# Performance work log

Measured on AMD Instinct MI355X. Metric: run time of the kernel, lower is better.

## Reference

```python
import jax, jax.numpy as jnp
import numpy as np

N, D, E = 100000, 128, 1600000
C = 1.0
MIN_NORM = 1e-15   # hgcn min_norm clamp
BALL_EPS = 4e-3    # float32 eps for proj onto Poincare ball


def artanh(x):
    # hgcn Artanh clamps input away from +-1 (use 1e-7, the fp32-representable analog of 1e-15)
    return jnp.arctanh(jnp.clip(x, -1.0 + 1e-7, 1.0 - 1e-7))


def _norm(x):
    return jnp.maximum(jnp.linalg.norm(x, axis=-1, keepdims=True), MIN_NORM)


def proj(x, c):
    norm = _norm(x)
    maxnorm = (1.0 - BALL_EPS) / jnp.sqrt(c)
    return jnp.where(norm > maxnorm, x / norm * maxnorm, x)


def expmap0(u, c):
    sc = jnp.sqrt(c)
    n = _norm(u)
    return jnp.tanh(sc * n) * u / (sc * n)


def logmap0(p, c):
    sc = jnp.sqrt(c)
    n = _norm(p)
    return artanh(sc * n) * p / (sc * n)


def mobius_add(x, y, c):
    x2 = jnp.sum(x * x, -1, keepdims=True)
    y2 = jnp.sum(y * y, -1, keepdims=True)
    xy = jnp.sum(x * y, -1, keepdims=True)
    num = (1.0 + 2.0 * c * xy + c * y2) * x + (1.0 - c * x2) * y
    den = 1.0 + 2.0 * c * xy + c * c * x2 * y2
    return num / jnp.maximum(den, MIN_NORM)


def mobius_matvec(m, x, c):
    sc = jnp.sqrt(c)
    xn = _norm(x)
    mx = x @ m.T
    mxn = _norm(mx)
    res = jnp.tanh(mxn / xn * artanh(sc * xn)) * mx / (mxn * sc)
    zero = jnp.all(mx == 0, axis=-1, keepdims=True)
    return jnp.where(zero, jnp.zeros_like(res), res)


def hgc_layer(x, edge_index, edge_weight, w, b, c_in, c_out, n):
    # HypLinear: mobius matvec + hyperbolic bias
    h = proj(mobius_matvec(w, x, c_in), c_in)
    hyp_b = proj(expmap0(b[None, :], c_in), c_in)
    h = proj(mobius_add(h, hyp_b, c_in), c_in)
    # HypAgg: aggregate in tangent space via sparse adjacency (spmm)
    xt = logmap0(h, c_in)                                   # [N, D]
    msg = xt[edge_index[1]] * edge_weight[:, None]          # [E, D]
    agg = jax.ops.segment_sum(msg, edge_index[0], num_segments=n)
    h = proj(expmap0(agg, c_in), c_in)
    # HypAct: relu in tangent space, re-map to ball at c_out
    xt = jax.nn.relu(logmap0(h, c_in))
    return proj(expmap0(xt, c_out), c_out)


def setup_inputs() -> dict:
    key = jax.random.key(0)
    ks = jax.random.split(key, 8)
    x = jax.random.normal(ks[0], (N, D), dtype=jnp.float32)
    edge_index = jax.random.randint(ks[1], (2, E), 0, N, dtype=jnp.int64 if jax.config.jax_enable_x64 else jnp.int32)
    edge_weight = jax.random.uniform(ks[2], (E,), dtype=jnp.float32)
    s = 1.0 / np.sqrt(D)
    w1 = jax.random.normal(ks[3], (D, D), dtype=jnp.float32) * s
    b1 = jax.random.normal(ks[4], (D,), dtype=jnp.float32) * s
    w2 = jax.random.normal(ks[5], (D, D), dtype=jnp.float32) * s
    b2 = jax.random.normal(ks[6], (D,), dtype=jnp.float32) * s
    return {"x": x, "edge_index": edge_index, "edge_weight": edge_weight,
            "w1": w1, "b1": b1, "w2": w2, "b2": b2}


def reference(x, edge_index, edge_weight, w1, b1, w2, b2):
    c = jnp.float32(C)
    n = x.shape[0]
    # encode(): proj_tan0 is identity on the Poincare ball
    xh = proj(expmap0(x, c), c)
    h = hgc_layer(xh, edge_index, edge_weight, w1, b1, c, c, n)
    h = hgc_layer(h, edge_index, edge_weight, w2, b2, c, c, n)
    return h
```

## Files before the change

kernel.cpp:

```cpp
#include <hip/hip_runtime.h>
#include <math.h>
#include <stdint.h>

#define D 128
#define MAXNORM (1.0f - 4e-3f)
#define ART_CLAMP 0.9999999f
#define BKT_BITS 7
#define BKT_NODES 128
#define BKT_CAP 4096
#define NB_ROWN 1024

typedef __attribute__((ext_vector_type(8))) short short8;
typedef __attribute__((ext_vector_type(4))) float float4v;
typedef __attribute__((ext_vector_type(4))) int intv4;

__device__ __forceinline__ float waveAllReduce(float v) {
#pragma unroll
    for (int off = 32; off; off >>= 1) v += __shfl_xor(v, off, 64);
    return v;
}

__device__ __forceinline__ float reduce16(float v) {
    v += __shfl_xor(v, 8, 64);
    v += __shfl_xor(v, 4, 64);
    v += __shfl_xor(v, 2, 64);
    v += __shfl_xor(v, 1, 64);
    return v;
}

__device__ __forceinline__ uint16_t f2bf(float f) {
    uint32_t u = __float_as_uint(f);
    uint32_t r = u + 0x7FFFu + ((u >> 16) & 1u);
    return (uint16_t)(r >> 16);
}
__device__ __forceinline__ float bf2f(uint16_t b) {
    return __uint_as_float((uint32_t)b << 16);
}

__device__ __forceinline__ float rcpf(float x) { return __builtin_amdgcn_rcpf(x); }
__device__ __forceinline__ float fsqrtf(float x) { return __builtin_amdgcn_sqrtf(x); }
__device__ __forceinline__ float fast_tanh(float x) {
    float e = __expf(2.0f * x);
    float t = 1.0f - 2.0f * rcpf(e + 1.0f);
    return (x < 1e-4f) ? x : t;
}
__device__ __forceinline__ float fast_atanh(float x) {
    float t = 0.5f * __logf((1.0f + x) * rcpf(1.0f - x));
    return (x < 1e-4f) ? x : t;
}


#define CS_STRIDE 136

struct GemmLds {
    short8 Ah[2][16][16];
    short8 Al[2][16][16];
    float Cs[16 * CS_STRIDE];
};
struct BinLds { int cnt[1024]; int base[1024]; };
struct SortLds { int cnt[BKT_NODES]; int cur[BKT_NODES]; int2 buf[BKT_CAP]; };
union LdsBG { GemmLds g; BinLds b; };
union LdsSG { GemmLds g; SortLds s; };


__device__ __forceinline__ void rowNorms_body(int bid, int tid,
                                              const float* __restrict__ X,
                                              float* __restrict__ XN, int n) {
    int lane = tid & 63;
    int wv = (bid * 256 + tid) >> 6;
    const int nw = (NB_ROWN * 256) >> 6;
    for (int r = wv; r < n; r += nw) {
        float2 v = *(const float2*)(X + (size_t)r * D + lane * 2);
        float nn = sqrtf(waveAllReduce(v.x * v.x + v.y * v.y));
        if (lane == 0) XN[r] = nn;
    }
}

__device__ __forceinline__ void histo_body(int bid, int tid,
                                           const int* __restrict__ DST,
                                           int* __restrict__ bcnt, int E, int B,
                                           int* cnt) {
    for (int i = tid; i < B; i += 256) cnt[i] = 0;
    __syncthreads();
    int start = bid * 8192;
    int endE = min(start + 8192, E);
    for (int e = start + tid; e < endE; e += 256)
        atomicAdd(&cnt[DST[e] >> BKT_BITS], 1);
    __syncthreads();
    for (int i = tid; i < B; i += 256)
        if (cnt[i]) atomicAdd(&bcnt[i], cnt[i]);
}

__device__ __forceinline__ void prepW_body(int bid, int tid,
                                           const float* __restrict__ W1,
                                           const float* __restrict__ W2,
                                           uint16_t* __restrict__ Whi1,
                                           uint16_t* __restrict__ Wlo1,
                                           uint16_t* __restrict__ Whi2,
                                           uint16_t* __restrict__ Wlo2) {
    int i = bid * 256 + tid;
    float a1 = W1[i];
    uint16_t h1 = f2bf(a1);
    Whi1[i] = h1;
    Wlo1[i] = f2bf(a1 - bf2f(h1));
    float a2 = W2[i];
    uint16_t h2 = f2bf(a2);
    Whi2[i] = h2;
    Wlo2[i] = f2bf(a2 - bf2f(h2));
}

__device__ __forceinline__ void bias_body(int bid, int tid,
                                          const float* __restrict__ B1,
                                          const float* __restrict__ B2,
                                          float* __restrict__ HBOUT) {
    if (tid >= 64) return;
    int lane = tid;
    const float* Bp = bid ? B2 : B1;
    float v0 = Bp[lane], v1 = Bp[lane + 64];
    float nn = fmaxf(sqrtf(waveAllReduce(v0 * v0 + v1 * v1)), 1e-15f);
    float t = tanhf(nn);
    float sc = t / nn;
    float pn = fmaxf(t, 1e-15f);
    if (pn > MAXNORM) sc *= MAXNORM / pn;
    HBOUT[bid * D + lane] = v0 * sc;
    HBOUT[bid * D + lane + 64] = v1 * sc;
}

__device__ __forceinline__ void binEdges_body(int bid, int tid,
                                              const int* __restrict__ DST,
                                              const int* __restrict__ SRC,
                                              const float* __restrict__ EW,
                                              int* __restrict__ gcur,
                                              int2* __restrict__ binned, int E, int B,
                                              int* cnt, int* base) {
    int start = bid * 8192;
    int endE = min(start + 8192, E);
    for (int i = tid; i < B; i += 256) cnt[i] = 0;
    __syncthreads();
    for (int e = start + tid; e < endE; e += 256)
        atomicAdd(&cnt[DST[e] >> BKT_BITS], 1);
    __syncthreads();
    for (int i = tid; i < B; i += 256) {
        int c = cnt[i];
        base[i] = (c > 0) ? atomicAdd(&gcur[i], c) : 0;
        cnt[i] = 0;
    }
    __syncthreads();
    for (int e = start + tid; e < endE; e += 256) {
        int d = DST[e];
        int bk = d >> BKT_BITS;
        int r = atomicAdd(&cnt[bk], 1);
        binned[base[bk] + r] =
            make_int2(SRC[e] | ((d & (BKT_NODES - 1)) << 24), __float_as_int(EW[e]));
    }
}

__device__ __forceinline__ void sort_body(int b, int tid,
                                          int2* __restrict__ binned,
                                          const int* __restrict__ boff,
                                          int* __restrict__ rp, int n,
                                          int* cnt, int* cur, int2* buf) {
    int beg = boff[b], end = boff[b + 1];
    if (tid < BKT_NODES) cnt[tid] = 0;
    __syncthreads();
    for (int e = beg + tid; e < end; e += 256)
        atomicAdd(&cnt[((uint32_t)binned[e].x) >> 24], 1);
    __syncthreads();
    int v = (tid < BKT_NODES) ? cnt[tid] : 0;
    if (tid < BKT_NODES) cur[tid] = v;
    __syncthreads();
    for (int off = 1; off < BKT_NODES; off <<= 1) {
        int t = (tid < BKT_NODES && tid >= off) ? cur[tid - off] : 0;
        __syncthreads();
        if (tid < BKT_NODES) cur[tid] += t;
        __syncthreads();
    }
    if (tid < BKT_NODES) {
        int ex = cur[tid] - v;
        int g = b * BKT_NODES + tid;
        if (g < n) rp[g] = beg + ex;
        cur[tid] = ex;
    }
    __syncthreads();
    for (int e = beg + tid; e < end; e += 256) {
        int2 pr = binned[e];
        int dl = ((uint32_t)pr.x) >> 24;
        int pos = atomicAdd(&cur[dl], 1);
        if (pos < BKT_CAP) buf[pos] = make_int2(pr.x & 0x00FFFFFF, pr.y);
    }
    __syncthreads();
    int cnt_tot = end - beg;
    for (int i = tid; i < cnt_tot && i < BKT_CAP; i += 256)
        binned[beg + i] = buf[i];
}


__device__ __forceinline__ void split8(const float* v, short8* hi, short8* lo) {
    union { uint32_t u[4]; short8 s; } H, L;
#pragma unroll
    for (int i = 0; i < 4; i++) {
        uint16_t h0 = f2bf(v[2 * i]), h1 = f2bf(v[2 * i + 1]);
        uint16_t l0 = f2bf(v[2 * i] - bf2f(h0));
        uint16_t l1 = f2bf(v[2 * i + 1] - bf2f(h1));
        H.u[i] = (uint32_t)h0 | ((uint32_t)h1 << 16);
        L.u[i] = (uint32_t)l0 | ((uint32_t)l1 << 16);
    }
    *hi = H.s;
    *lo = L.s;
}

template <bool ENCODE>
__device__ __forceinline__ void gemm_body(int gbid, int rowOff, int tid,
                                          const float* __restrict__ A,
                                          const uint16_t* __restrict__ Whi,
                                          const uint16_t* __restrict__ Wlo,
                                          const float* __restrict__ XN,
                                          const float* __restrict__ HB,
                                          uint16_t* __restrict__ XT, int n,
                                          GemmLds* L) {
    int lane = tid & 63;
    int wv = tid >> 6;
    int tx = lane & 15;
    int q = lane >> 4;
    int sw = tx & 7;
    int row0 = rowOff + gbid * 64;

    short8 wh[2][4], wl[2][4];
#pragma unroll
    for (int c = 0; c < 2; c++) {
        int wrow = 16 * (2 * wv + c) + tx;
        const uint16_t* ph = Whi + (size_t)wrow * D + q * 8;
        const uint16_t* pl = Wlo + (size_t)wrow * D + q * 8;
#pragma unroll
        for (int t = 0; t < 4; t++) {
            wh[c][t] = *(const short8*)(ph + t * 32);
            wl[c][t] = *(const short8*)(pl + t * 32);
        }
    }

    float hbf[8];
#pragma unroll
    for (int c = 0; c < 8; c++) hbf[c] = HB[16 * c + tx];
    float hbsq = 0.f;
#pragma unroll
    for (int c = 0; c < 8; c++) hbsq += hbf[c] * hbf[c];
    float hb2 = reduce16(hbsq);

    auto loadA = [&](int tau, float4& v0, float4& v1) {
        int gr = row0 + tau * 16 + tx;
        if (gr >= n) gr = n - 1;
        const float4* ap = (const float4*)(A + (size_t)gr * D + wv * 32 + q * 8);
        v0 = ap[0];
        v1 = ap[1];
    };
    auto splitStore = [&](int b, float4 v0, float4 v1) {
        float v[8] = {v0.x, v0.y, v0.z, v0.w, v1.x, v1.y, v1.z, v1.w};
        short8 hi, lo;
        split8(v, &hi, &lo);
        int pch = (4 * wv + q) ^ sw;
        L->Ah[b][tx][pch] = hi;
        L->Al[b][tx][pch] = lo;
    };

    float4 pa0, pa1;
    loadA(0, pa0, pa1);
    splitStore(0, pa0, pa1);
    loadA(1, pa0, pa1);
    __syncthreads();

#pragma unroll
    for (int tau = 0; tau < 4; tau++) {
        int b = tau & 1;
        float4v acc[2];
        acc[0] = (float4v){0.f, 0.f, 0.f, 0.f};
        acc[1] = (float4v){0.f, 0.f, 0.f, 0.f};
#pragma unroll
        for (int t = 0; t < 4; t++) {
            int pch = (4 * t + q) ^ sw;
            short8 ahi = L->Ah[b][tx][pch];
            short8 alo = L->Al[b][tx][pch];
#pragma unroll
            for (int c = 0; c < 2; c++) {
                acc[c] = __builtin_amdgcn_mfma_f32_16x16x32_bf16(ahi, wh[c][t], acc[c], 0, 0, 0);
                acc[c] = __builtin_amdgcn_mfma_f32_16x16x32_bf16(ahi, wl[c][t], acc[c], 0, 0, 0);
                acc[c] = __builtin_amdgcn_mfma_f32_16x16x32_bf16(alo, wh[c][t], acc[c], 0, 0, 0);
            }
        }

#pragma unroll
        for (int c = 0; c < 2; c++) {
            int col = 16 * (2 * wv + c) + tx;
#pragma unroll
            for (int p = 0; p < 4; p++) {
                int lr = 4 * q + p;
                L->Cs[lr * CS_STRIDE + ((col + 4 * lr) & 127)] = acc[c][p];
            }
        }

        if (tau < 3) {
            splitStore(b ^ 1, pa0, pa1);
            if (tau < 2) loadA(tau + 2, pa0, pa1);
        }
        __syncthreads();

        int lr = 4 * wv + q;
        int row = row0 + tau * 16 + lr;
        if (row < n) {
            float y[8];
#pragma unroll
            for (int c = 0; c < 8; c++)
                y[c] = L->Cs[lr * CS_STRIDE + ((16 * c + tx + 4 * lr) & 127)];

            float s = 0.f;
#pragma unroll
            for (int c = 0; c < 8; c++) s += y[c] * y[c];
            float yn2 = reduce16(s);
            float sc, xns;
            if (ENCODE) {
                float nn = fmaxf(XN[row], 1e-15f);
                float t = fast_tanh(nn);
                sc = t * rcpf(nn);
                float pn = fmaxf(t, 1e-15f);
                if (pn > MAXNORM) { sc *= MAXNORM * rcpf(pn); pn = MAXNORM; }
                xns = pn;
            } else {
                sc = 1.0f;
                xns = fmaxf(XN[row], 1e-15f);
            }
            float mxn2 = sc * sc * yn2;
            float mxn = fmaxf(fsqrtf(mxn2), 1e-15f);
            float arg = (mxn * rcpf(xns)) * fast_atanh(fminf(xns, ART_CLAMP));
            float t = fast_tanh(arg);
            float s2 = (mxn2 == 0.0f) ? 0.0f : (sc * t * rcpf(mxn));
            float h[8];
#pragma unroll
            for (int c = 0; c < 8; c++) h[c] = y[c] * s2;
            float rn = fmaxf(t, 1e-15f);
            float hn = rn;
            if (rn > MAXNORM) {
                float f = MAXNORM * rcpf(rn);
#pragma unroll
                for (int c = 0; c < 8; c++) h[c] *= f;
                hn = MAXNORM;
            }
            float x2 = hn * hn;
            float d0 = 0.f;
#pragma unroll
            for (int c = 0; c < 8; c++) d0 += h[c] * hbf[c];
            float xy = reduce16(d0);
            float k1 = 1.0f + 2.0f * xy + hb2;
            float k2 = 1.0f - x2;
            float den = fmaxf(1.0f + 2.0f * xy + x2 * hb2, 1e-15f);
            float rden = rcpf(den);
            float av[8];
            float s3 = 0.f;
#pragma unroll
            for (int c = 0; c < 8; c++) {
                av[c] = (k1 * h[c] + k2 * hbf[c]) * rden;
                s3 += av[c] * av[c];
            }
            float an = fmaxf(fsqrtf(reduce16(s3)), 1e-15f);
            float fproj = 1.0f;
            if (an > MAXNORM) { fproj = MAXNORM * rcpf(an); an = MAXNORM; }
            float lm = fproj * fast_atanh(fminf(an, ART_CLAMP)) * rcpf(an);
            uint16_t* o = XT + (size_t)row * D + tx;
#pragma unroll
            for (int c = 0; c < 8; c++) o[16 * c] = f2bf(av[c] * lm);
        }
        __syncthreads();
    }
}


__global__ __launch_bounds__(256) void fusedPre(
    const float* __restrict__ X, float* __restrict__ XN, int n,
    const int* __restrict__ DST, int* __restrict__ bcnt, int E, int B, int gH,
    const float* __restrict__ W1, const float* __restrict__ W2,
    uint16_t* __restrict__ Whi1, uint16_t* __restrict__ Wlo1,
    uint16_t* __restrict__ Whi2, uint16_t* __restrict__ Wlo2,
    const float* __restrict__ B1, const float* __restrict__ B2,
    float* __restrict__ HBOUT) {
    __shared__ int cnt[1024];
    int bid = blockIdx.x, tid = threadIdx.x;
    if (bid < NB_ROWN) {
        rowNorms_body(bid, tid, X, XN, n);
    } else if (bid < NB_ROWN + gH) {
        histo_body(bid - NB_ROWN, tid, DST, bcnt, E, B, cnt);
    } else if (bid < NB_ROWN + gH + 64) {
        prepW_body(bid - NB_ROWN - gH, tid, W1, W2, Whi1, Wlo1, Whi2, Wlo2);
    } else {
        bias_body(bid - NB_ROWN - gH - 64, tid, B1, B2, HBOUT);
    }
}

__global__ __launch_bounds__(1024) void bucketScan(const int* __restrict__ bcnt,
                                                   int* __restrict__ boff,
                                                   int* __restrict__ gcur,
                                                   int* __restrict__ rp_last,
                                                   int B, int E) {
    __shared__ int sd[1024];
    int tid = threadIdx.x;
    int v = (tid < B) ? bcnt[tid] : 0;
    sd[tid] = v;
    __syncthreads();
    for (int off = 1; off < 1024; off <<= 1) {
        int t = (tid >= off) ? sd[tid - off] : 0;
        __syncthreads();
        sd[tid] += t;
        __syncthreads();
    }
    int ex = sd[tid] - v;
    if (tid < B) { boff[tid] = ex; gcur[tid] = ex; }
    if (tid == 0) { boff[B] = E; *rp_last = E; }
}

__global__ __launch_bounds__(256, 3) void fusedBinGemm(
    const int* __restrict__ DST, const int* __restrict__ SRC,
    const float* __restrict__ EW, int* __restrict__ gcur,
    int2* __restrict__ binned, int E, int B, int gBin,
    const float* __restrict__ A, const uint16_t* __restrict__ Whi,
    const uint16_t* __restrict__ Wlo, const float* __restrict__ XN,
    const float* __restrict__ HB, uint16_t* __restrict__ XT, int n) {
    __shared__ LdsBG u;
    int bid = blockIdx.x, tid = threadIdx.x;
    if (bid < gBin)
        binEdges_body(bid, tid, DST, SRC, EW, gcur, binned, E, B, u.b.cnt, u.b.base);
    else
        gemm_body<true>(bid - gBin, 0, tid, A, Whi, Wlo, XN, HB, XT, n, &u.g);
}

__global__ __launch_bounds__(256, 3) void fusedSortGemm(
    int2* __restrict__ binned, const int* __restrict__ boff,
    int* __restrict__ rp, int n, int gSort,
    const float* __restrict__ A, const uint16_t* __restrict__ Whi,
    const uint16_t* __restrict__ Wlo, const float* __restrict__ XN,
    const float* __restrict__ HB, uint16_t* __restrict__ XT, int rowOff) {
    __shared__ LdsSG u;
    int bid = blockIdx.x, tid = threadIdx.x;
    if (bid < gSort)
        sort_body(bid, tid, binned, boff, rp, n, u.s.cnt, u.s.cur, u.s.buf);
    else
        gemm_body<true>(bid - gSort, rowOff, tid, A, Whi, Wlo, XN, HB, XT, n, &u.g);
}

template <bool ENCODE>
__global__ __launch_bounds__(256, 3) void gemmM(const float* __restrict__ A,
                                                const uint16_t* __restrict__ Whi,
                                                const uint16_t* __restrict__ Wlo,
                                                const float* __restrict__ XN,
                                                const float* __restrict__ HB,
                                                uint16_t* __restrict__ XT, int n) {
    __shared__ GemmLds L;
    gemm_body<ENCODE>(blockIdx.x, 0, threadIdx.x, A, Whi, Wlo, XN, HB, XT, n, &L);
}


template <bool STORE_HN>
__global__ __launch_bounds__(256) void aggC(const uint16_t* __restrict__ XT,
                                            const int* __restrict__ rp,
                                            const int2* __restrict__ sorted,
                                            float* __restrict__ OUT,
                                            float* __restrict__ HN, int n) {
    int tid = threadIdx.x;
    int lane = tid & 63;
    int q = lane >> 4;
    int tx = lane & 15;
    int wv = (blockIdx.x * 256 + tid) >> 6;
    int g = wv * 4 + q;
    bool valid = (g < n);
    int gc = valid ? g : (n - 1);
    uint32_t beg = (uint32_t)rp[gc];
    uint32_t end = valid ? (uint32_t)rp[gc + 1] : beg;
    uint32_t deg = end - beg;

    int m = (int)deg;
    m = max(m, __shfl_xor(m, 16, 64));
    m = max(m, __shfl_xor(m, 32, 64));
    int ms = __builtin_amdgcn_readfirstlane(m);

    const char* sbase = (const char*)sorted;
    const char* xbase = (const char*)XT;
    uint32_t txoff = (uint32_t)tx * 16u;
    uint32_t jb = beg * 8u;
    uint32_t jendb = end * 8u;
    uint32_t jlastb = (jendb > 0u) ? (jendb - 8u) : 0u;

    float a[8];
#pragma unroll
    for (int c = 0; c < 8; c++) a[c] = 0.f;

    int2 e0 = *(const int2*)(sbase + min(jb, jlastb));
    int2 e1 = *(const int2*)(sbase + min(jb + 8u, jlastb));
    int2 e2 = *(const int2*)(sbase + min(jb + 16u, jlastb));
    int2 e3 = *(const int2*)(sbase + min(jb + 24u, jlastb));
    for (int i = 0; i < ms; i += 4) {
        int2 f0 = *(const int2*)(sbase + min(jb + 32u, jlastb));
        int2 f1 = *(const int2*)(sbase + min(jb + 40u, jlastb));
        int2 f2 = *(const int2*)(sbase + min(jb + 48u, jlastb));
        int2 f3 = *(const int2*)(sbase + min(jb + 56u, jlastb));
        intv4 u0 = *(const intv4*)(xbase + ((((uint32_t)e0.x) << 8) + txoff));
        intv4 u1 = *(const intv4*)(xbase + ((((uint32_t)e1.x) << 8) + txoff));
        intv4 u2 = *(const intv4*)(xbase + ((((uint32_t)e2.x) << 8) + txoff));
        intv4 u3 = *(const intv4*)(xbase + ((((uint32_t)e3.x) << 8) + txoff));
        float w0 = (jb < jendb) ? __int_as_float(e0.y) : 0.f;
        float w1 = (jb + 8u < jendb) ? __int_as_float(e1.y) : 0.f;
        float w2 = (jb + 16u < jendb) ? __int_as_float(e2.y) : 0.f;
        float w3 = (jb + 24u < jendb) ? __int_as_float(e3.y) : 0.f;
#pragma unroll
        for (int k = 0; k < 4; k++) {
            a[2 * k]     = fmaf(__uint_as_float(((uint32_t)u0[k]) << 16), w0, a[2 * k]);
            a[2 * k + 1] = fmaf(__uint_as_float(((uint32_t)u0[k]) & 0xFFFF0000u), w0, a[2 * k + 1]);
        }
#pragma unroll
        for (int k = 0; k < 4; k++) {
            a[2 * k]     = fmaf(__uint_as_float(((uint32_t)u1[k]) << 16), w1, a[2 * k]);
            a[2 * k + 1] = fmaf(__uint_as_float(((uint32_t)u1[k]) & 0xFFFF0000u), w1, a[2 * k + 1]);
        }
#pragma unroll
        for (int k = 0; k < 4; k++) {
            a[2 * k]     = fmaf(__uint_as_float(((uint32_t)u2[k]) << 16), w2, a[2 * k]);
            a[2 * k + 1] = fmaf(__uint_as_float(((uint32_t)u2[k]) & 0xFFFF0000u), w2, a[2 * k + 1]);
        }
#pragma unroll
        for (int k = 0; k < 4; k++) {
            a[2 * k]     = fmaf(__uint_as_float(((uint32_t)u3[k]) << 16), w3, a[2 * k]);
            a[2 * k + 1] = fmaf(__uint_as_float(((uint32_t)u3[k]) & 0xFFFF0000u), w3, a[2 * k + 1]);
        }
        jb += 32u;
        e0 = f0; e1 = f1; e2 = f2; e3 = f3;
    }

    float ss = 0.f;
#pragma unroll
    for (int c = 0; c < 8; c++) ss += a[c] * a[c];
    float nn = fmaxf(fsqrtf(reduce16(ss)), 1e-15f);
    float t = fast_tanh(nn);
    float sc = t * rcpf(nn);
    float pn = fmaxf(t, 1e-15f);
    if (pn > MAXNORM) { sc *= MAXNORM * rcpf(pn); pn = MAXNORM; }
    float lm = fast_atanh(fminf(pn, ART_CLAMP)) * rcpf(pn);
    float r[8];
    float ss2 = 0.f;
#pragma unroll
    for (int c = 0; c < 8; c++) {
        r[c] = fmaxf(lm * sc * a[c], 0.f);
        ss2 += r[c] * r[c];
    }
    float rn = fmaxf(fsqrtf(reduce16(ss2)), 1e-15f);
    float t2 = fast_tanh(rn);
    float sc2 = t2 * rcpf(rn);
    float on = fmaxf(t2, 1e-15f);
    if (on > MAXNORM) { sc2 *= MAXNORM * rcpf(on); on = MAXNORM; }
    if (valid) {
        float4* o = (float4*)(OUT + (size_t)g * D + tx * 8);
        o[0] = make_float4(r[0] * sc2, r[1] * sc2, r[2] * sc2, r[3] * sc2);
        o[1] = make_float4(r[4] * sc2, r[5] * sc2, r[6] * sc2, r[7] * sc2);
        if (STORE_HN && tx == 0) HN[g] = on;
    }
}


extern "C" void kernel_launch(void* const* d_in, const int* in_sizes, int n_in,
                              void* d_out, int out_size, void* d_ws, size_t ws_size,
                              hipStream_t stream) {
    const float* x  = (const float*)d_in[0];
    const int*   ei = (const int*)d_in[1];
    const float* ew = (const float*)d_in[2];
    const float* w1 = (const float*)d_in[3];
    const float* b1 = (const float*)d_in[4];
    const float* w2 = (const float*)d_in[5];
    const float* b2 = (const float*)d_in[6];
    int n = in_sizes[0] / D;
    int E = in_sizes[2];
    int B = (n + BKT_NODES - 1) >> BKT_BITS;

    uint16_t* xtb = (uint16_t*)d_ws;
    int*   bcnt = (int*)(xtb + (size_t)n * D);
    int*   boff = bcnt + 1024;
    int*   gcur = boff + 1025;
    int*   rp   = gcur + 1024;
    float* xn   = (float*)(rp + n + 1);
    uint16_t* whi1 = (uint16_t*)(((uintptr_t)(xn + n) + 15) & ~(uintptr_t)15);
    uint16_t* wlo1 = whi1 + 128 * 128;
    uint16_t* whi2 = wlo1 + 128 * 128;
    uint16_t* wlo2 = whi2 + 128 * 128;
    float* hb = (float*)(wlo2 + 128 * 128);
    uintptr_t p = (uintptr_t)(hb + 2 * D);
    int2* binned = (int2*)((p + 15) & ~(uintptr_t)15);
    float* Hd = (float*)d_out;

    const int* dst = ei;
    const int* src = ei + E;

    const int gE8 = (E + 8191) / 8192;
    const int gG = (n + 63) / 64;
    const int GA = min(256, gG);
    const int GB = gG - GA;
    const int gAgg = (n + 15) / 16;

    hipMemsetAsync(bcnt, 0, 1024 * sizeof(int), stream);

    fusedPre<<<NB_ROWN + gE8 + 64 + 2, 256, 0, stream>>>(
        x, xn, n, dst, bcnt, E, B, gE8,
        w1, w2, whi1, wlo1, whi2, wlo2, b1, b2, hb);

    bucketScan<<<1, 1024, 0, stream>>>(bcnt, boff, gcur, rp + n, B, E);

    fusedBinGemm<<<gE8 + GA, 256, 0, stream>>>(
        dst, src, ew, gcur, binned, E, B, gE8,
        x, whi1, wlo1, xn, hb, xtb, n);

    fusedSortGemm<<<B + GB, 256, 0, stream>>>(
        binned, boff, rp, n, B,
        x, whi1, wlo1, xn, hb, xtb, GA * 64);

    aggC<true><<<gAgg, 256, 0, stream>>>(xtb, rp, binned, Hd, xn, n);
    gemmM<false><<<gG, 256, 0, stream>>>(Hd, whi2, wlo2, xn, hb + D, xtb, n);
    aggC<false><<<gAgg, 256, 0, stream>>>(xtb, rp, binned, (float*)d_out, nullptr, n);
}
```

Before: 382.7 us.

## Store per-block bucket histograms and precompute bin offsets instead of recounting

The histogram pass now writes each block's per-bucket counts to global memory, with a rotated start offset to spread out the global atomics. A new small scan kernel turns these into per-block base offsets. The binning pass then reads those bases directly instead of re-histogramming DST and taking base slots with global atomics on gcur. This removes a full pass over DST and the atomic contention in binning, at the cost of an extra kernel launch and a serial per-bucket loop over ~196 blocks.

```diff
diff --git a/kernel.cpp b/kernel.cpp
--- a/kernel.cpp
+++ b/kernel.cpp
@@ -78,7 +78,8 @@
 
 __device__ __forceinline__ void histo_body(int bid, int tid,
                                            const int* __restrict__ DST,
-                                           int* __restrict__ bcnt, int E, int B,
+                                           int* __restrict__ bcnt,
+                                           int* __restrict__ Hcnt, int E, int B,
                                            int* cnt) {
     for (int i = tid; i < B; i += 256) cnt[i] = 0;
     __syncthreads();
@@ -87,8 +88,14 @@
     for (int e = start + tid; e < endE; e += 256)
         atomicAdd(&cnt[DST[e] >> BKT_BITS], 1);
     __syncthreads();
-    for (int i = tid; i < B; i += 256)
-        if (cnt[i]) atomicAdd(&bcnt[i], cnt[i]);
+    int off = (bid * 131) % B;
+    for (int i = tid; i < B; i += 256) {
+        int j = i + off;
+        if (j >= B) j -= B;
+        int c = cnt[j];
+        Hcnt[bid * B + j] = c;
+        if (c) atomicAdd(&bcnt[j], c);
+    }
 }
 
 __device__ __forceinline__ void prepW_body(int bid, int tid,
@@ -130,22 +137,16 @@
                                               const int* __restrict__ DST,
                                               const int* __restrict__ SRC,
                                               const float* __restrict__ EW,
-                                              int* __restrict__ gcur,
+                                              const int* __restrict__ Hbase,
                                               int2* __restrict__ binned, int E, int B,
                                               int* cnt, int* base) {
+    for (int i = tid; i < B; i += 256) {
+        base[i] = Hbase[bid * B + i];
+        cnt[i] = 0;
+    }
+    __syncthreads();
     int start = bid * 8192;
     int endE = min(start + 8192, E);
-    for (int i = tid; i < B; i += 256) cnt[i] = 0;
-    __syncthreads();
-    for (int e = start + tid; e < endE; e += 256)
-        atomicAdd(&cnt[DST[e] >> BKT_BITS], 1);
-    __syncthreads();
-    for (int i = tid; i < B; i += 256) {
-        int c = cnt[i];
-        base[i] = (c > 0) ? atomicAdd(&gcur[i], c) : 0;
-        cnt[i] = 0;
-    }
-    __syncthreads();
     for (int e = start + tid; e < endE; e += 256) {
         int d = DST[e];
         int bk = d >> BKT_BITS;
@@ -374,7 +375,8 @@
 
 __global__ __launch_bounds__(256) void fusedPre(
     const float* __restrict__ X, float* __restrict__ XN, int n,
-    const int* __restrict__ DST, int* __restrict__ bcnt, int E, int B, int gH,
+    const int* __restrict__ DST, int* __restrict__ bcnt, int* __restrict__ Hcnt,
+    int E, int B, int gH,
     const float* __restrict__ W1, const float* __restrict__ W2,
     uint16_t* __restrict__ Whi1, uint16_t* __restrict__ Wlo1,
     uint16_t* __restrict__ Whi2, uint16_t* __restrict__ Wlo2,
@@ -385,7 +387,7 @@
     if (bid < NB_ROWN) {
         rowNorms_body(bid, tid, X, XN, n);
     } else if (bid < NB_ROWN + gH) {
-        histo_body(bid - NB_ROWN, tid, DST, bcnt, E, B, cnt);
+        histo_body(bid - NB_ROWN, tid, DST, bcnt, Hcnt, E, B, cnt);
     } else if (bid < NB_ROWN + gH + 64) {
         prepW_body(bid - NB_ROWN - gH, tid, W1, W2, Whi1, Wlo1, Whi2, Wlo2);
     } else {
@@ -395,7 +397,6 @@
 
 __global__ __launch_bounds__(1024) void bucketScan(const int* __restrict__ bcnt,
                                                    int* __restrict__ boff,
-                                                   int* __restrict__ gcur,
                                                    int* __restrict__ rp_last,
                                                    int B, int E) {
     __shared__ int sd[1024];
@@ -410,13 +411,25 @@
         __syncthreads();
     }
     int ex = sd[tid] - v;
-    if (tid < B) { boff[tid] = ex; gcur[tid] = ex; }
+    if (tid < B) boff[tid] = ex;
     if (tid == 0) { boff[B] = E; *rp_last = E; }
+}
+
+__global__ __launch_bounds__(256) void scanA(const int* __restrict__ boff,
+                                             const int* __restrict__ Hcnt,
+                                             int* __restrict__ Hbase, int B, int gH) {
+    int b = blockIdx.x * 256 + threadIdx.x;
+    if (b >= B) return;
+    int run = boff[b];
+    for (int k = 0; k < gH; k++) {
+        Hbase[k * B + b] = run;
+        run += Hcnt[k * B + b];
+    }
 }
 
 __global__ __launch_bounds__(256, 3) void fusedBinGemm(
     const int* __restrict__ DST, const int* __restrict__ SRC,
-    const float* __restrict__ EW, int* __restrict__ gcur,
+    const float* __restrict__ EW, const int* __restrict__ Hbase,
     int2* __restrict__ binned, int E, int B, int gBin,
     const float* __restrict__ A, const uint16_t* __restrict__ Whi,
     const uint16_t* __restrict__ Wlo, const float* __restrict__ XN,
@@ -424,7 +437,7 @@
     __shared__ LdsBG u;
     int bid = blockIdx.x, tid = threadIdx.x;
     if (bid < gBin)
-        binEdges_body(bid, tid, DST, SRC, EW, gcur, binned, E, B, u.b.cnt, u.b.base);
+        binEdges_body(bid, tid, DST, SRC, EW, Hbase, binned, E, B, u.b.cnt, u.b.base);
     else
         gemm_body<true>(bid - gBin, 0, tid, A, Whi, Wlo, XN, HB, XT, n, &u.g);
 }
@@ -593,6 +606,9 @@
     const int* src = ei + E;
 
     const int gE8 = (E + 8191) / 8192;
+    int* Hcnt  = (int*)(binned + E);
+    int* Hbase = Hcnt + (size_t)gE8 * B;
+
     const int gG = (n + 63) / 64;
     const int GA = min(256, gG);
     const int GB = gG - GA;
@@ -601,13 +617,15 @@
     hipMemsetAsync(bcnt, 0, 1024 * sizeof(int), stream);
 
     fusedPre<<<NB_ROWN + gE8 + 64 + 2, 256, 0, stream>>>(
-        x, xn, n, dst, bcnt, E, B, gE8,
+        x, xn, n, dst, bcnt, Hcnt, E, B, gE8,
         w1, w2, whi1, wlo1, whi2, wlo2, b1, b2, hb);
 
-    bucketScan<<<1, 1024, 0, stream>>>(bcnt, boff, gcur, rp + n, B, E);
+    bucketScan<<<1, 1024, 0, stream>>>(bcnt, boff, rp + n, B, E);
+
+    scanA<<<(B + 255) / 256, 256, 0, stream>>>(boff, Hcnt, Hbase, B, gE8);
 
     fusedBinGemm<<<gE8 + GA, 256, 0, stream>>>(
-        dst, src, ew, gcur, binned, E, B, gE8,
+        dst, src, ew, Hbase, binned, E, B, gE8,
         x, whi1, wlo1, xn, hb, xtb, n);
 
     fusedSortGemm<<<B + GB, 256, 0, stream>>>(
```

Result: slower. 418.5 us (+9.4%).
